# Kernel optimization log

Hardware: AMD Instinct MI355X
Metric: run time of the kernel (lower is better)

Reference implementation:

```python
import jax, jax.numpy as jnp
import numpy as np

N_NODES, N_EDGES, EMB_DIM = 100000, 1000000, 64
NUM_BOND_TYPE, NUM_BOND_DIR = 6, 3  # self-loop bond type index = 4


def gcn_conv(x, src, dst, bond_type, bond_dir, W, b, emb_bond, emb_dir):
    """One GCNConv (Hu et al. mol-GNN variant). src/dst/attrs already include self-loops."""
    N = x.shape[0]
    edge_emb = emb_bond[bond_type] + emb_dir[bond_dir]           # [Etot, D]
    ones = jnp.ones(src.shape[0], x.dtype)
    deg = jax.ops.segment_sum(ones, src, num_segments=N)         # scatter_add over row
    dis = jnp.where(deg > 0, jax.lax.rsqrt(deg), 0.0)
    norm = dis[src] * dis[dst]                                   # [Etot]
    h = x @ W.T + b                                              # [N, D]
    msg = norm[:, None] * (h[src] + edge_emb)                    # [Etot, D]
    return jax.ops.segment_sum(msg, dst, num_segments=N)         # add-aggregate at target


def with_self_loops(edge_index, edge_attr, N):
    loop = jnp.arange(N, dtype=edge_index.dtype)
    src = jnp.concatenate([edge_index[0], loop])
    dst = jnp.concatenate([edge_index[1], loop])
    bt = jnp.concatenate([edge_attr[:, 0], jnp.full((N,), 4, edge_attr.dtype)])
    bd = jnp.concatenate([edge_attr[:, 1], jnp.zeros((N,), edge_attr.dtype)])
    return src, dst, bt, bd


def setup_inputs() -> dict:
    key = jax.random.key(0)
    ks = jax.random.split(key, 12)
    D = EMB_DIM
    s = 1.0 / np.sqrt(D)
    inp = {
        "x": jax.random.normal(ks[0], (N_NODES, D), jnp.float32),
        "edge_index": jax.random.randint(ks[1], (2, N_EDGES), 0, N_NODES, jnp.int64 if jax.config.jax_enable_x64 else jnp.int32),
        "edge_attr": jax.random.randint(ks[2], (N_EDGES, 2), 0, 3, jnp.int64 if jax.config.jax_enable_x64 else jnp.int32),
        "W1": jax.random.uniform(ks[3], (D, D), jnp.float32, -s, s),
        "b1": jax.random.uniform(ks[4], (D,), jnp.float32, -s, s),
        "ebond1": jax.random.normal(ks[5], (NUM_BOND_TYPE, D), jnp.float32) * 0.1,
        "edir1": jax.random.normal(ks[6], (NUM_BOND_DIR, D), jnp.float32) * 0.1,
        "W2": jax.random.uniform(ks[7], (D, D), jnp.float32, -s, s),
        "b2": jax.random.uniform(ks[8], (D,), jnp.float32, -s, s),
        "ebond2": jax.random.normal(ks[9], (NUM_BOND_TYPE, D), jnp.float32) * 0.1,
        "edir2": jax.random.normal(ks[10], (NUM_BOND_DIR, D), jnp.float32) * 0.1,
    }
    return inp


def reference(x, edge_index, edge_attr, W1, b1, ebond1, edir1, W2, b2, ebond2, edir2):
    N = x.shape[0]
    src, dst, bt, bd = with_self_loops(edge_index, edge_attr, N)
    h = gcn_conv(x, src, dst, bt, bd, W1, b1, ebond1, edir1)
    h = jax.nn.relu(h)
    out = gcn_conv(h, src, dst, bt, bd, W2, b2, ebond2, edir2)
    return out
```

## Files before the change

### kernel.cpp

```cpp
#include <hip/hip_runtime.h>


#define THREADS 256
#define MAXNB 128
#define BCAP 16384
#define SCAP 4096
#define CHUNK 4096
#define GEMM_SMEM_BYTES (64 * 68 * 4)
#define SC_SMEM (4 * CHUNK * 2 + CHUNK * 2 + 9 * 128 * 4)

typedef __attribute__((ext_vector_type(8))) short bf16x8;
typedef __attribute__((ext_vector_type(4))) float f32x4;

__device__ __forceinline__ float bflo(unsigned int v) { return __uint_as_float(v << 16); }
__device__ __forceinline__ float bfhi(unsigned int v) { return __uint_as_float(v & 0xFFFF0000u); }
__device__ __forceinline__ unsigned short f2bf(float f) {
    unsigned int u = __float_as_uint(f);
    return (unsigned short)((u + 0x7FFFu + ((u >> 16) & 1u)) >> 16);
}
__device__ __forceinline__ int sb(unsigned int w, int j) {
    return (int)(w << (24 - 8 * j)) >> 24;
}

template <bool XBF16>
__device__ __forceinline__ void gemm64_body(int tile, const void* __restrict__ Xv,
                                            const float* __restrict__ W,
                                            const float* __restrict__ B,
                                            unsigned short* __restrict__ Hb,
                                            unsigned char* __restrict__ Hq,
                                            float2* __restrict__ dsc, int N,
                                            float (*smem)[68]) {
    int t = threadIdx.x;
    int lane = t & 63;
    int wave = __builtin_amdgcn_readfirstlane(t >> 6);
    int l15 = lane & 15;
    int lk = lane >> 4;
    int arow = tile * 64 + wave * 16 + l15;

    bf16x8 a0, a1;
    if (arow < N) {
        if (XBF16) {
            const unsigned short* xp = (const unsigned short*)Xv + (size_t)arow * 64 + 8 * lk;
            a0 = *(const bf16x8*)xp;
            a1 = *(const bf16x8*)(xp + 32);
        } else {
            const float* xp = (const float*)Xv + (size_t)arow * 64 + 8 * lk;
            float4 v0 = *(const float4*)xp;
            float4 v1 = *(const float4*)(xp + 4);
            float4 v2 = *(const float4*)(xp + 32);
            float4 v3 = *(const float4*)(xp + 36);
            a0[0] = (short)f2bf(v0.x); a0[1] = (short)f2bf(v0.y);
            a0[2] = (short)f2bf(v0.z); a0[3] = (short)f2bf(v0.w);
            a0[4] = (short)f2bf(v1.x); a0[5] = (short)f2bf(v1.y);
            a0[6] = (short)f2bf(v1.z); a0[7] = (short)f2bf(v1.w);
            a1[0] = (short)f2bf(v2.x); a1[1] = (short)f2bf(v2.y);
            a1[2] = (short)f2bf(v2.z); a1[3] = (short)f2bf(v2.w);
            a1[4] = (short)f2bf(v3.x); a1[5] = (short)f2bf(v3.y);
            a1[6] = (short)f2bf(v3.z); a1[7] = (short)f2bf(v3.w);
        }
    } else {
#pragma unroll
        for (int e = 0; e < 8; ++e) { a0[e] = 0; a1[e] = 0; }
    }

    bf16x8 bfr[4][2];
#pragma unroll
    for (int n = 0; n < 4; ++n) {
        const float* wp = W + (size_t)(16 * n + l15) * 64 + 8 * lk;
#pragma unroll
        for (int ks = 0; ks < 2; ++ks) {
            float4 u0 = *(const float4*)(wp + 32 * ks);
            float4 u1 = *(const float4*)(wp + 32 * ks + 4);
            bf16x8 bb;
            bb[0] = (short)f2bf(u0.x); bb[1] = (short)f2bf(u0.y);
            bb[2] = (short)f2bf(u0.z); bb[3] = (short)f2bf(u0.w);
            bb[4] = (short)f2bf(u1.x); bb[5] = (short)f2bf(u1.y);
            bb[6] = (short)f2bf(u1.z); bb[7] = (short)f2bf(u1.w);
            bfr[n][ks] = bb;
        }
    }

    f32x4 acc[4];
#pragma unroll
    for (int n = 0; n < 4; ++n) {
        f32x4 z = {0.0f, 0.0f, 0.0f, 0.0f};
        z = __builtin_amdgcn_mfma_f32_16x16x32_bf16(a0, bfr[n][0], z, 0, 0, 0);
        acc[n] = __builtin_amdgcn_mfma_f32_16x16x32_bf16(a1, bfr[n][1], z, 0, 0, 0);
    }

#pragma unroll
    for (int n = 0; n < 4; ++n) {
        float bv = B[16 * n + l15];
        int col = 16 * n + l15;
#pragma unroll
        for (int r = 0; r < 4; ++r)
            smem[16 * wave + 4 * lk + r][col] = acc[n][r] + bv;
    }
    __syncthreads();

#pragma unroll
    for (int i = 0; i < 2; ++i) {
        int idx = t + i * THREADS;
        int r = idx >> 3;
        int c8 = (idx & 7) << 3;
        int grow = tile * 64 + r;
        float4 va = *(const float4*)(&smem[r][c8]);
        float4 vb = *(const float4*)(&smem[r][c8 + 4]);
        float v[8] = {va.x, va.y, va.z, va.w, vb.x, vb.y, vb.z, vb.w};
        float m = fabsf(v[0]);
#pragma unroll
        for (int j = 1; j < 8; ++j) m = fmaxf(m, fabsf(v[j]));
        m = fmaxf(m, __shfl_xor(m, 1));
        m = fmaxf(m, __shfl_xor(m, 2));
        m = fmaxf(m, __shfl_xor(m, 4));
        if (grow < N) {
            uint4 o;
            o.x = (unsigned)f2bf(v[0]) | ((unsigned)f2bf(v[1]) << 16);
            o.y = (unsigned)f2bf(v[2]) | ((unsigned)f2bf(v[3]) << 16);
            o.z = (unsigned)f2bf(v[4]) | ((unsigned)f2bf(v[5]) << 16);
            o.w = (unsigned)f2bf(v[6]) | ((unsigned)f2bf(v[7]) << 16);
            *(uint4*)(Hb + (size_t)grow * 64 + c8) = o;
            float inv = m > 0.0f ? 127.0f / m : 0.0f;
            int q[8];
#pragma unroll
            for (int j = 0; j < 8; ++j) q[j] = __float2int_rn(v[j] * inv);
            uint2 qp;
            qp.x = (unsigned)(q[0] & 255) | ((unsigned)(q[1] & 255) << 8) |
                   ((unsigned)(q[2] & 255) << 16) | ((unsigned)(q[3] & 255) << 24);
            qp.y = (unsigned)(q[4] & 255) | ((unsigned)(q[5] & 255) << 8) |
                   ((unsigned)(q[6] & 255) << 16) | ((unsigned)(q[7] & 255) << 24);
            *(uint2*)(Hq + (size_t)grow * 64 + c8) = qp;
            if ((idx & 7) == 0) dsc[grow].y = m * (1.0f / 127.0f);
        }
    }
}

__global__ __launch_bounds__(THREADS) void zero_gemm_kernel(
    int* __restrict__ gcur, int ncur, const float* __restrict__ X,
    const float* __restrict__ W1, const float* __restrict__ B1,
    unsigned short* __restrict__ Hb, unsigned char* __restrict__ Hq,
    float2* __restrict__ dsc, int N, int tile0) {
    __shared__ __align__(16) char sh[GEMM_SMEM_BYTES];
    int b = blockIdx.x;
    if (b == 0) {
        for (int i = threadIdx.x; i < ncur; i += THREADS) gcur[i] = 0;
        return;
    }
    gemm64_body<false>(tile0 + b - 1, X, W1, B1, Hb, Hq, dsc, N, (float(*)[68])sh);
}

__global__ __launch_bounds__(THREADS) void scatter_kernel(
    const int* __restrict__ src, const int* __restrict__ dst, const int* __restrict__ attr,
    int* __restrict__ gcurS, int* __restrict__ gcurD, unsigned short* __restrict__ payS,
    unsigned int* __restrict__ payD, int E, int SCB,
    const float* __restrict__ X, const float* __restrict__ W1, const float* __restrict__ B1,
    unsigned short* __restrict__ Hb, unsigned char* __restrict__ Hq,
    float2* __restrict__ dsc, int N, int tile0) {
    __shared__ __align__(16) char sh[SC_SMEM];
    int b = blockIdx.x;
    if (b >= SCB) {
        gemm64_body<false>(tile0 + b - SCB, X, W1, B1, Hb, Hq, dsc, N, (float(*)[68])sh);
        return;
    }
    unsigned int* Wv  = (unsigned int*)sh;
    unsigned int* SD  = Wv + CHUNK;
    unsigned char* DB = (unsigned char*)(SD + CHUNK);
    unsigned char* SDB = DB + CHUNK;
    int* hD   = (int*)(SDB + CHUNK);
    int* hS   = hD + 128;
    int* loD  = hS + 128;
    int* loS  = loD + 128;
    int* mapD = loS + 128;
    int* mapS = mapD + 128;
    int* curD = mapS + 128;
    int* curS = curD + 128;
    int* scn  = curS + 128;
    unsigned short* SS = (unsigned short*)Wv;
    unsigned char* SSB = DB;

    int t = threadIdx.x;
    if (t < 128) { hD[t] = 0; hS[t] = 0; }
    __syncthreads();

    int lo = b * CHUNK, hi = min(E, lo + CHUNK);
    int nch = hi - lo;
    const int2* ap = (const int2*)attr;
    for (int li = t; li < nch; li += THREADS) {
        int i = lo + li;
        int sv = src[i], dv = dst[i];
        int2 a = ap[i];
        Wv[li] = (unsigned int)sv | ((unsigned int)(a.x * 3 + a.y) << 17) |
                 ((unsigned int)(dv & 1023) << 22);
        DB[li] = (unsigned char)(dv >> 10);
        atomicAdd(&hD[dv >> 10], 1);
        atomicAdd(&hS[sv >> 10], 1);
    }
    __syncthreads();

    if (t < 128) {
        int h = hD[t];
        int r = h ? atomicAdd(&gcurD[t], h) : 0;
        mapD[t] = t * BCAP + r;
        int h2 = hS[t];
        int r2 = h2 ? atomicAdd(&gcurS[t], h2) : 0;
        mapS[t] = t * BCAP + r2;
    }
    if (t < 128) scn[t] = hD[t];
    __syncthreads();
    for (int d = 1; d < 128; d <<= 1) {
        int a = (t >= d && t < 128) ? scn[t - d] : 0;
        __syncthreads();
        if (t < 128) scn[t] += a;
        __syncthreads();
    }
    if (t < 128) {
        int e = scn[t] - hD[t];
        loD[t] = e;
        curD[t] = e;
        mapD[t] -= e;
        scn[t] = hS[t];
    }
    __syncthreads();
    for (int d = 1; d < 128; d <<= 1) {
        int a = (t >= d && t < 128) ? scn[t - d] : 0;
        __syncthreads();
        if (t < 128) scn[t] += a;
        __syncthreads();
    }
    if (t < 128) {
        int e = scn[t] - hS[t];
        loS[t] = e;
        curS[t] = e;
        mapS[t] -= e;
    }
    __syncthreads();

    for (int li = t; li < nch; li += THREADS) {
        int k = DB[li];
        int p = atomicAdd(&curD[k], 1);
        SD[p] = Wv[li];
        SDB[p] = (unsigned char)k;
    }
    __syncthreads();

    for (int li = t; li < nch; li += THREADS) {
        int val = (int)(SD[li] & 0x1FFFFu);
        int k = val >> 10;
        int p = atomicAdd(&curS[k], 1);
        SS[p] = (unsigned short)(val & 1023);
        SSB[p] = (unsigned char)k;
    }
    __syncthreads();

    for (int li = t; li < nch; li += THREADS) {
        payD[mapD[SDB[li]] + li] = SD[li];
        payS[mapS[SSB[li]] + li] = SS[li];
    }
}

__global__ __launch_bounds__(THREADS) void build_kernel(
    const unsigned short* __restrict__ payS, const unsigned int* __restrict__ payD,
    const int* __restrict__ gcurS, const int* __restrict__ gcurD,
    unsigned int* __restrict__ sorted, int* __restrict__ row_ptr, int* __restrict__ cnt_out,
    int NB, const float* __restrict__ X, const float* __restrict__ W1,
    const float* __restrict__ B1, unsigned short* __restrict__ Hb,
    unsigned char* __restrict__ Hq, float2* __restrict__ dsc, int N, int tile0) {
    __shared__ __align__(16) char sh[GEMM_SMEM_BYTES];
    int b = blockIdx.x;
    if (b >= 8 * NB) {
        gemm64_body<false>(tile0 + b - 8 * NB, X, W1, B1, Hb, Hq, dsc, N, (float(*)[68])sh);
        return;
    }
    int t = threadIdx.x;
    if (b < 4 * NB) {
        int k = b >> 2, j = b & 3;
        int* cnt = (int*)sh;
        cnt[t] = 0;
        __syncthreads();
        int n = gcurS[k], off = k * BCAP;
        for (int i = t; i < n; i += THREADS) {
            int val = payS[off + i];
            if ((val >> 8) == j) atomicAdd(&cnt[val & 255], 1);
        }
        __syncthreads();
        int node = k * 1024 + j * 256 + t;
        if (node < N) dsc[node].x = 1.0f / sqrtf(1.0f + (float)cnt[t]);
    } else {
        int b2 = b - 4 * NB;
        int k = b2 >> 2, j = b2 & 3;
        int* cnt = (int*)sh;
        int* cur = cnt + 256;
        int* s = cur + 256;
        cnt[t] = 0;
        __syncthreads();
        int ecnt = gcurD[k], eoff = k * BCAP;
        for (int i = t; i < ecnt; i += THREADS) {
            unsigned int d10 = payD[eoff + i] >> 22;
            if ((int)(d10 >> 8) == j) atomicAdd(&cnt[d10 & 255], 1);
        }
        __syncthreads();
        int v = cnt[t];
        s[t] = v;
        __syncthreads();
        for (int d = 1; d < THREADS; d <<= 1) {
            int a = (t >= d) ? s[t - d] : 0;
            __syncthreads();
            s[t] += a;
            __syncthreads();
        }
        int excl = s[t] - v;
        int obase = (4 * k + j) * SCAP;
        int node = k * 1024 + j * 256 + t;
        if (node < N) {
            row_ptr[node] = obase + excl;
            cnt_out[node] = v;
        }
        cur[t] = excl;
        __syncthreads();
        for (int i = t; i < ecnt; i += THREADS) {
            unsigned int u = payD[eoff + i];
            unsigned int d10 = u >> 22;
            if ((int)(d10 >> 8) == j) {
                int p = atomicAdd(&cur[d10 & 255], 1);
                sorted[obase + p] = u & 0x3FFFFFu;
            }
        }
    }
}

template <bool XBF16>
__global__ __launch_bounds__(THREADS) void gemm64_kernel(const void* __restrict__ Xv,
                                                         const float* __restrict__ W,
                                                         const float* __restrict__ B,
                                                         unsigned short* __restrict__ Hb,
                                                         unsigned char* __restrict__ Hq,
                                                         float2* __restrict__ dsc, int N) {
    __shared__ __align__(16) char sh[GEMM_SMEM_BYTES];
    gemm64_body<XBF16>(blockIdx.x, Xv, W, B, Hb, Hq, dsc, N, (float(*)[68])sh);
}

__device__ __forceinline__ void edge_acc(unsigned int u, float dn,
                                         const float2* __restrict__ dsc,
                                         const unsigned char* __restrict__ Hq, int c,
                                         const float (*embc)[64], float acc[8]) {
    int s0 = u & 0x1FFFF;
    int e0 = (u >> 17) & 31;
    float2 ds = dsc[s0];
    uint2 q = *(const uint2*)(Hq + (size_t)s0 * 64 + c);
    float w = ds.x * dn, ws = w * ds.y;
    float4 ea = *(const float4*)(&embc[e0][c]);
    float4 eb = *(const float4*)(&embc[e0][c + 4]);
    acc[0] = fmaf(ws, (float)sb(q.x, 0), fmaf(w, ea.x, acc[0]));
    acc[1] = fmaf(ws, (float)sb(q.x, 1), fmaf(w, ea.y, acc[1]));
    acc[2] = fmaf(ws, (float)sb(q.x, 2), fmaf(w, ea.z, acc[2]));
    acc[3] = fmaf(ws, (float)sb(q.x, 3), fmaf(w, ea.w, acc[3]));
    acc[4] = fmaf(ws, (float)sb(q.y, 0), fmaf(w, eb.x, acc[4]));
    acc[5] = fmaf(ws, (float)sb(q.y, 1), fmaf(w, eb.y, acc[5]));
    acc[6] = fmaf(ws, (float)sb(q.y, 2), fmaf(w, eb.z, acc[6]));
    acc[7] = fmaf(ws, (float)sb(q.y, 3), fmaf(w, eb.w, acc[7]));
}

template <bool RELU_BF16_OUT>
__global__ __launch_bounds__(THREADS) void aggregate_kernel(
    const unsigned short* __restrict__ Hb, const unsigned char* __restrict__ Hq,
    const float2* __restrict__ dsc, const float* __restrict__ ebond,
    const float* __restrict__ edir, const int* __restrict__ row_ptr,
    const int* __restrict__ cnt, const unsigned int* __restrict__ entries,
    void* __restrict__ outv, int N) {
    __shared__ float embc[18][64];
    int t = threadIdx.x;
    for (int i = t; i < 18 * 64; i += THREADS) {
        int row = i >> 6, c = i & 63;
        embc[row][c] = ebond[(row / 3) * 64 + c] + edir[(row % 3) * 64 + c];
    }
    __syncthreads();

    int n = blockIdx.x * 32 + (t >> 3);
    if (n >= N) return;
    int c = (t & 7) << 3;

    float dn = dsc[n].x;
    uint4 hv = *(const uint4*)(Hb + (size_t)n * 64 + c);
    float4 ea = *(const float4*)(&embc[12][c]);
    float4 eb = *(const float4*)(&embc[12][c + 4]);
    float nrm = dn * dn;
    float accA[8], accB[8];
    accA[0] = nrm * (bflo(hv.x) + ea.x);
    accA[1] = nrm * (bfhi(hv.x) + ea.y);
    accA[2] = nrm * (bflo(hv.y) + ea.z);
    accA[3] = nrm * (bfhi(hv.y) + ea.w);
    accA[4] = nrm * (bflo(hv.z) + eb.x);
    accA[5] = nrm * (bfhi(hv.z) + eb.y);
    accA[6] = nrm * (bflo(hv.w) + eb.z);
    accA[7] = nrm * (bfhi(hv.w) + eb.w);
#pragma unroll
    for (int j = 0; j < 8; ++j) accB[j] = 0.0f;

    int p = row_ptr[n];
    int end = p + cnt[n];
    const float(*ec)[64] = (const float(*)[64])embc;
    for (; p + 3 < end; p += 4) {
        unsigned int u0 = entries[p];
        unsigned int u1 = entries[p + 1];
        unsigned int u2 = entries[p + 2];
        unsigned int u3 = entries[p + 3];
        edge_acc(u0, dn, dsc, Hq, c, ec, accA);
        edge_acc(u1, dn, dsc, Hq, c, ec, accB);
        edge_acc(u2, dn, dsc, Hq, c, ec, accA);
        edge_acc(u3, dn, dsc, Hq, c, ec, accB);
    }
    for (; p < end; ++p) edge_acc(entries[p], dn, dsc, Hq, c, ec, accA);

    float o[8];
#pragma unroll
    for (int j = 0; j < 8; ++j) o[j] = accA[j] + accB[j];

    if (RELU_BF16_OUT) {
        unsigned short* ob = (unsigned short*)outv;
        uint4 ov;
        ov.x = (unsigned)f2bf(fmaxf(o[0], 0.0f)) | ((unsigned)f2bf(fmaxf(o[1], 0.0f)) << 16);
        ov.y = (unsigned)f2bf(fmaxf(o[2], 0.0f)) | ((unsigned)f2bf(fmaxf(o[3], 0.0f)) << 16);
        ov.z = (unsigned)f2bf(fmaxf(o[4], 0.0f)) | ((unsigned)f2bf(fmaxf(o[5], 0.0f)) << 16);
        ov.w = (unsigned)f2bf(fmaxf(o[6], 0.0f)) | ((unsigned)f2bf(fmaxf(o[7], 0.0f)) << 16);
        *(uint4*)(ob + (size_t)n * 64 + c) = ov;
    } else {
        float* of = (float*)outv;
        *(float4*)(of + (size_t)n * 64 + c) = make_float4(o[0], o[1], o[2], o[3]);
        *(float4*)(of + (size_t)n * 64 + c + 4) = make_float4(o[4], o[5], o[6], o[7]);
    }
}

extern "C" void kernel_launch(void* const* d_in, const int* in_sizes, int n_in,
                              void* d_out, int out_size, void* d_ws, size_t ws_size,
                              hipStream_t stream) {
    const float* x      = (const float*)d_in[0];
    const int*   eidx   = (const int*)d_in[1];
    const int*   eattr  = (const int*)d_in[2];
    const float* W1     = (const float*)d_in[3];
    const float* b1     = (const float*)d_in[4];
    const float* ebond1 = (const float*)d_in[5];
    const float* edir1  = (const float*)d_in[6];
    const float* W2     = (const float*)d_in[7];
    const float* b2     = (const float*)d_in[8];
    const float* ebond2 = (const float*)d_in[9];
    const float* edir2  = (const float*)d_in[10];

    const int N = in_sizes[0] / 64;
    const int E = in_sizes[1] / 2;
    const int* src = eidx;
    const int* dst = eidx + E;
    float* out = (float*)d_out;
    const int NB = (N + 1023) >> 10;
    const int SCB = (E + CHUNK - 1) / CHUNK;

    char* w = (char*)d_ws;
    size_t Na = ((size_t)N * 4 + 255) & ~(size_t)255;
    float2* dsc    = (float2*)w;           w += 2 * Na;
    int*   row_ptr = (int*)w;              w += Na;
    int*   cnt     = (int*)w;              w += Na;
    int*   gcur    = (int*)w;              w += 2 * MAXNB * 4;
    unsigned int* payD   = (unsigned int*)w;   w += (size_t)MAXNB * BCAP * 4;
    unsigned int* sorted = (unsigned int*)w;   w += (size_t)4 * MAXNB * SCAP * 4;
    unsigned short* payS = (unsigned short*)w; w += (size_t)MAXNB * BCAP * 2;
    unsigned short* Hb   = (unsigned short*)w; w += (size_t)N * 64 * 2;
    unsigned char*  Hq   = (unsigned char*)w;  w += ((size_t)N * 64 + 255) & ~(size_t)255;
    unsigned short* Ab   = (unsigned short*)w; w += (size_t)N * 64 * 2;
    int* gcurS = gcur;
    int* gcurD = gcur + MAXNB;

    const int gT   = (N + 63) / 64;
    const int gN32 = (N + 31) / 32;

    const int t0 = min(gT, 256);
    const int t1 = min(gT - t0, 512);
    const int t2 = gT - t0 - t1;

    zero_gemm_kernel<<<1 + t0, THREADS, 0, stream>>>(gcur, 2 * MAXNB, x, W1, b1, Hb, Hq,
                                                     dsc, N, 0);
    scatter_kernel<<<SCB + t1, THREADS, 0, stream>>>(src, dst, eattr, gcurS, gcurD, payS,
                                                     payD, E, SCB, x, W1, b1, Hb, Hq,
                                                     dsc, N, t0);
    build_kernel<<<8 * NB + t2, THREADS, 0, stream>>>(payS, payD, gcurS, gcurD, sorted,
                                                      row_ptr, cnt, NB, x, W1, b1, Hb, Hq,
                                                      dsc, N, t0 + t1);

    aggregate_kernel<true><<<gN32, THREADS, 0, stream>>>(Hb, Hq, dsc, ebond1, edir1, row_ptr,
                                                         cnt, sorted, Ab, N);

    gemm64_kernel<true><<<gT, THREADS, 0, stream>>>(Ab, W2, b2, Hb, Hq, dsc, N);
    aggregate_kernel<false><<<gN32, THREADS, 0, stream>>>(Hb, Hq, dsc, ebond2, edir2, row_ptr,
                                                          cnt, sorted, out, N);
}
```

Measured before the change: 230.9 us.

## Build CSR per 1024-node bucket with LDS staging instead of four sub-blocks

The build kernel now uses one block per 1024-node bucket instead of four 256-node sub-blocks. Each block counts all 1024 nodes, scans four values per thread, and stages the sorted edges in shared memory before a coalesced write-out. This removes the 4x redundant reads of each bucket's payload and the filtering. The GEMM tiles that previously overlapped with the build kernel move into the zero and scatter kernels, and BCAP shrinks to 12288. In exchange, build has only 2*NB blocks, which gives low parallelism and needs about 58KB of LDS per block. The smaller BCAP also risks overflow on skewed inputs.

```diff
diff --git a/kernel.cpp b/kernel.cpp
--- a/kernel.cpp
+++ b/kernel.cpp
@@ -3,11 +3,11 @@
 
 #define THREADS 256
 #define MAXNB 128
-#define BCAP 16384
-#define SCAP 4096
+#define BCAP 12288
 #define CHUNK 4096
 #define GEMM_SMEM_BYTES (64 * 68 * 4)
-#define SC_SMEM (4 * CHUNK * 2 + CHUNK * 2 + 9 * 128 * 4)
+#define SC_SMEM (CHUNK * 4 * 2 + CHUNK * 2 + 7 * MAXNB * 4)
+#define BD_SMEM ((1024 + 1024 + 256 + BCAP) * 4)
 
 typedef __attribute__((ext_vector_type(8))) short bf16x8;
 typedef __attribute__((ext_vector_type(4))) float f32x4;
@@ -152,7 +152,7 @@
 __global__ __launch_bounds__(THREADS) void scatter_kernel(
     const int* __restrict__ src, const int* __restrict__ dst, const int* __restrict__ attr,
     int* __restrict__ gcurS, int* __restrict__ gcurD, unsigned short* __restrict__ payS,
-    unsigned int* __restrict__ payD, int E, int SCB,
+    unsigned int* __restrict__ payD, int E, int NB, int SCB,
     const float* __restrict__ X, const float* __restrict__ W1, const float* __restrict__ B1,
     unsigned short* __restrict__ Hb, unsigned char* __restrict__ Hq,
     float2* __restrict__ dsc, int N, int tile0) {
@@ -162,24 +162,22 @@
         gemm64_body<false>(tile0 + b - SCB, X, W1, B1, Hb, Hq, dsc, N, (float(*)[68])sh);
         return;
     }
-    unsigned int* Wv  = (unsigned int*)sh;
-    unsigned int* SD  = Wv + CHUNK;
+    unsigned int* Wv = (unsigned int*)sh;
+    unsigned int* SD = Wv + CHUNK;
     unsigned char* DB = (unsigned char*)(SD + CHUNK);
     unsigned char* SDB = DB + CHUNK;
-    int* hD   = (int*)(SDB + CHUNK);
-    int* hS   = hD + 128;
-    int* loD  = hS + 128;
-    int* loS  = loD + 128;
-    int* mapD = loS + 128;
-    int* mapS = mapD + 128;
-    int* curD = mapS + 128;
-    int* curS = curD + 128;
-    int* scn  = curS + 128;
+    int* hD = (int*)(SDB + CHUNK);
+    int* hS = hD + MAXNB;
+    int* mapD = hS + MAXNB;
+    int* mapS = mapD + MAXNB;
+    int* curD = mapS + MAXNB;
+    int* curS = curD + MAXNB;
+    int* scn = curS + MAXNB;
     unsigned short* SS = (unsigned short*)Wv;
     unsigned char* SSB = DB;
 
     int t = threadIdx.x;
-    if (t < 128) { hD[t] = 0; hS[t] = 0; }
+    if (t < MAXNB) { hD[t] = 0; hS[t] = 0; }
     __syncthreads();
 
     int lo = b * CHUNK, hi = min(E, lo + CHUNK);
@@ -197,7 +195,7 @@
     }
     __syncthreads();
 
-    if (t < 128) {
+    if (t < NB) {
         int h = hD[t];
         int r = h ? atomicAdd(&gcurD[t], h) : 0;
         mapD[t] = t * BCAP + r;
@@ -205,33 +203,32 @@
         int r2 = h2 ? atomicAdd(&gcurS[t], h2) : 0;
         mapS[t] = t * BCAP + r2;
     }
-    if (t < 128) scn[t] = hD[t];
-    __syncthreads();
-    for (int d = 1; d < 128; d <<= 1) {
-        int a = (t >= d && t < 128) ? scn[t - d] : 0;
-        __syncthreads();
-        if (t < 128) scn[t] += a;
-        __syncthreads();
-    }
-    if (t < 128) {
-        int e = scn[t] - hD[t];
-        loD[t] = e;
-        curD[t] = e;
-        mapD[t] -= e;
-        scn[t] = hS[t];
-    }
-    __syncthreads();
-    for (int d = 1; d < 128; d <<= 1) {
-        int a = (t >= d && t < 128) ? scn[t - d] : 0;
-        __syncthreads();
-        if (t < 128) scn[t] += a;
-        __syncthreads();
-    }
-    if (t < 128) {
-        int e = scn[t] - hS[t];
-        loS[t] = e;
-        curS[t] = e;
-        mapS[t] -= e;
+    if (t < MAXNB) scn[t] = (t < NB) ? hD[t] : 0;
+    __syncthreads();
+    for (int d = 1; d < MAXNB; d <<= 1) {
+        int a = (t >= d && t < MAXNB) ? scn[t - d] : 0;
+        __syncthreads();
+        if (t < MAXNB) scn[t] += a;
+        __syncthreads();
+    }
+    if (t < NB) {
+        int excl = scn[t] - hD[t];
+        curD[t] = excl;
+        mapD[t] -= excl;
+    }
+    __syncthreads();
+    if (t < MAXNB) scn[t] = (t < NB) ? hS[t] : 0;
+    __syncthreads();
+    for (int d = 1; d < MAXNB; d <<= 1) {
+        int a = (t >= d && t < MAXNB) ? scn[t - d] : 0;
+        __syncthreads();
+        if (t < MAXNB) scn[t] += a;
+        __syncthreads();
+    }
+    if (t < NB) {
+        int excl = scn[t] - hS[t];
+        curS[t] = excl;
+        mapS[t] -= excl;
     }
     __syncthreads();
 
@@ -262,45 +259,36 @@
     const unsigned short* __restrict__ payS, const unsigned int* __restrict__ payD,
     const int* __restrict__ gcurS, const int* __restrict__ gcurD,
     unsigned int* __restrict__ sorted, int* __restrict__ row_ptr, int* __restrict__ cnt_out,
-    int NB, const float* __restrict__ X, const float* __restrict__ W1,
-    const float* __restrict__ B1, unsigned short* __restrict__ Hb,
-    unsigned char* __restrict__ Hq, float2* __restrict__ dsc, int N, int tile0) {
-    __shared__ __align__(16) char sh[GEMM_SMEM_BYTES];
+    int NB, float2* __restrict__ dsc, int N) {
+    __shared__ __align__(16) char sh[BD_SMEM];
+    int* cnt = (int*)sh;
+    int* cur = cnt + 1024;
+    int* s = cur + 1024;
+    unsigned int* stg = (unsigned int*)(s + 256);
+    int t = threadIdx.x;
     int b = blockIdx.x;
-    if (b >= 8 * NB) {
-        gemm64_body<false>(tile0 + b - 8 * NB, X, W1, B1, Hb, Hq, dsc, N, (float(*)[68])sh);
-        return;
-    }
-    int t = threadIdx.x;
-    if (b < 4 * NB) {
-        int k = b >> 2, j = b & 3;
-        int* cnt = (int*)sh;
-        cnt[t] = 0;
+    if (b < NB) {
+        int k = b;
+        for (int i = t; i < 1024; i += THREADS) cnt[i] = 0;
         __syncthreads();
         int n = gcurS[k], off = k * BCAP;
-        for (int i = t; i < n; i += THREADS) {
-            int val = payS[off + i];
-            if ((val >> 8) == j) atomicAdd(&cnt[val & 255], 1);
-        }
-        __syncthreads();
-        int node = k * 1024 + j * 256 + t;
-        if (node < N) dsc[node].x = 1.0f / sqrtf(1.0f + (float)cnt[t]);
+        for (int i = t; i < n; i += THREADS) atomicAdd(&cnt[payS[off + i]], 1);
+        __syncthreads();
+        for (int i = t; i < 1024; i += THREADS) {
+            int node = k * 1024 + i;
+            if (node < N) dsc[node].x = 1.0f / sqrtf(1.0f + (float)cnt[i]);
+        }
     } else {
-        int b2 = b - 4 * NB;
-        int k = b2 >> 2, j = b2 & 3;
-        int* cnt = (int*)sh;
-        int* cur = cnt + 256;
-        int* s = cur + 256;
-        cnt[t] = 0;
+        int k = b - NB;
+        for (int i = t; i < 1024; i += THREADS) cnt[i] = 0;
         __syncthreads();
         int ecnt = gcurD[k], eoff = k * BCAP;
-        for (int i = t; i < ecnt; i += THREADS) {
-            unsigned int d10 = payD[eoff + i] >> 22;
-            if ((int)(d10 >> 8) == j) atomicAdd(&cnt[d10 & 255], 1);
-        }
-        __syncthreads();
-        int v = cnt[t];
-        s[t] = v;
+        for (int i = t; i < ecnt; i += THREADS)
+            atomicAdd(&cnt[(payD[eoff + i] >> 22) & 1023], 1);
+        __syncthreads();
+        int base4 = t * 4;
+        int v0 = cnt[base4], v1 = cnt[base4 + 1], v2 = cnt[base4 + 2], v3 = cnt[base4 + 3];
+        s[t] = v0 + v1 + v2 + v3;
         __syncthreads();
         for (int d = 1; d < THREADS; d <<= 1) {
             int a = (t >= d) ? s[t - d] : 0;
@@ -308,23 +296,29 @@
             s[t] += a;
             __syncthreads();
         }
-        int excl = s[t] - v;
-        int obase = (4 * k + j) * SCAP;
-        int node = k * 1024 + j * 256 + t;
-        if (node < N) {
-            row_ptr[node] = obase + excl;
-            cnt_out[node] = v;
-        }
-        cur[t] = excl;
+        int off = (t == 0) ? 0 : s[t - 1];
+        int o0 = off, o1 = off + v0, o2 = o1 + v1, o3 = o2 + v2;
+        __syncthreads();
+        cur[base4] = o0;
+        cur[base4 + 1] = o1;
+        cur[base4 + 2] = o2;
+        cur[base4 + 3] = o3;
+#pragma unroll
+        for (int j = 0; j < 4; ++j) {
+            int node = k * 1024 + base4 + j;
+            if (node < N) {
+                row_ptr[node] = eoff + ((j == 0) ? o0 : (j == 1) ? o1 : (j == 2) ? o2 : o3);
+                cnt_out[node] = (j == 0) ? v0 : (j == 1) ? v1 : (j == 2) ? v2 : v3;
+            }
+        }
         __syncthreads();
         for (int i = t; i < ecnt; i += THREADS) {
             unsigned int u = payD[eoff + i];
-            unsigned int d10 = u >> 22;
-            if ((int)(d10 >> 8) == j) {
-                int p = atomicAdd(&cur[d10 & 255], 1);
-                sorted[obase + p] = u & 0x3FFFFFu;
-            }
-        }
+            int p = atomicAdd(&cur[(u >> 22) & 1023], 1);
+            stg[p] = u & 0x3FFFFFu;
+        }
+        __syncthreads();
+        for (int i = t; i < ecnt; i += THREADS) sorted[eoff + i] = stg[i];
     }
 }
 
@@ -460,7 +454,7 @@
     int*   cnt     = (int*)w;              w += Na;
     int*   gcur    = (int*)w;              w += 2 * MAXNB * 4;
     unsigned int* payD   = (unsigned int*)w;   w += (size_t)MAXNB * BCAP * 4;
-    unsigned int* sorted = (unsigned int*)w;   w += (size_t)4 * MAXNB * SCAP * 4;
+    unsigned int* sorted = (unsigned int*)w;   w += (size_t)MAXNB * BCAP * 4;
     unsigned short* payS = (unsigned short*)w; w += (size_t)MAXNB * BCAP * 2;
     unsigned short* Hb   = (unsigned short*)w; w += (size_t)N * 64 * 2;
     unsigned char*  Hq   = (unsigned char*)w;  w += ((size_t)N * 64 + 255) & ~(size_t)255;
@@ -471,18 +465,16 @@
     const int gT   = (N + 63) / 64;
     const int gN32 = (N + 31) / 32;
 
-    const int t0 = min(gT, 256);
-    const int t1 = min(gT - t0, 512);
-    const int t2 = gT - t0 - t1;
+    const int t0 = min(gT, 512);
+    const int t1 = gT - t0;
 
     zero_gemm_kernel<<<1 + t0, THREADS, 0, stream>>>(gcur, 2 * MAXNB, x, W1, b1, Hb, Hq,
                                                      dsc, N, 0);
     scatter_kernel<<<SCB + t1, THREADS, 0, stream>>>(src, dst, eattr, gcurS, gcurD, payS,
-                                                     payD, E, SCB, x, W1, b1, Hb, Hq,
+                                                     payD, E, NB, SCB, x, W1, b1, Hb, Hq,
                                                      dsc, N, t0);
-    build_kernel<<<8 * NB + t2, THREADS, 0, stream>>>(payS, payD, gcurS, gcurD, sorted,
-                                                      row_ptr, cnt, NB, x, W1, b1, Hb, Hq,
-                                                      dsc, N, t0 + t1);
+    build_kernel<<<2 * NB, THREADS, 0, stream>>>(payS, payD, gcurS, gcurD, sorted,
+                                                 row_ptr, cnt, NB, dsc, N);
 
     aggregate_kernel<true><<<gN32, THREADS, 0, stream>>>(Hb, Hq, dsc, ebond1, edir1, row_ptr,
                                                          cnt, sorted, Ab, N);
```

Result: faster. 224.8 us (-2.7%).
